# Kernel tuning notes

Hardware: AMD Instinct MI355X
Metric: run time of the kernel (lower is better)

## Reference

```python
import jax, jax.numpy as jnp
import numpy as np

B, L, D = 2, 1024, 768
NL = 8            # n_layers
DI = 2 * D        # d_inner (expand=2)
NS = 16           # d_state
DR = D // 16      # dt_rank = 48
KC = 4            # d_conv
EPS = 1e-5


def setup_inputs() -> dict:
    key = jax.random.key(0)
    ks = jax.random.split(key, 12)
    s = 0.02
    inp = {
        "x":        jax.random.normal(ks[0], (B, L, D), jnp.float32),
        "ln_w":     jnp.ones((NL, D), jnp.float32),
        "ln_b":     jnp.zeros((NL, D), jnp.float32),
        "in_proj":  jax.random.normal(ks[1], (NL, 2 * DI, D), jnp.float32) * s,
        "conv_w":   jax.random.normal(ks[2], (NL, DI, KC), jnp.float32) * 0.1,
        "conv_b":   jnp.zeros((NL, DI), jnp.float32),
        "x_proj":   jax.random.normal(ks[3], (NL, DR + 2 * NS, DI), jnp.float32) * s,
        "dt_w":     jax.random.normal(ks[4], (NL, DI, DR), jnp.float32) * s,
        "dt_b":     jax.random.normal(ks[5], (NL, DI), jnp.float32) * 0.5,
        "A_log":    jnp.broadcast_to(jnp.log(jnp.arange(1, NS + 1, dtype=jnp.float32)), (NL, DI, NS)).copy(),
        "D_skip":   jnp.ones((NL, DI), jnp.float32),
        "out_proj": jax.random.normal(ks[6], (NL, D, DI), jnp.float32) * s,
        "fn_w":     jnp.ones((D,), jnp.float32),
        "fn_b":     jnp.zeros((D,), jnp.float32),
    }
    return inp


def _layernorm(x, w, b):
    mu = x.mean(-1, keepdims=True)
    var = ((x - mu) ** 2).mean(-1, keepdims=True)
    return (x - mu) * jax.lax.rsqrt(var + EPS) * w + b


def _silu(x):
    return x * jax.nn.sigmoid(x)


def _mamba(xn, Wi, cw, cb, Wx, Wdt, bdt, A_log, Dp, Wo):
    # xn: (B, L, D)
    xz = jnp.einsum('bld,ed->ble', xn, Wi)          # (B, L, 2*DI)
    xi, z = jnp.split(xz, 2, axis=-1)               # each (B, L, DI)
    # causal depthwise conv along L
    xc = jax.lax.conv_general_dilated(
        xi.transpose(0, 2, 1), cw[:, None, :], (1,), [(KC - 1, 0)],
        feature_group_count=DI, dimension_numbers=('NCH', 'OIH', 'NCH'))
    xc = _silu(xc.transpose(0, 2, 1) + cb)          # (B, L, DI)
    dbc = jnp.einsum('ble,re->blr', xc, Wx)         # (B, L, DR+2*NS)
    dt = jax.nn.softplus(jnp.einsum('blr,dr->bld', dbc[..., :DR], Wdt) + bdt)  # (B,L,DI)
    Bm = dbc[..., DR:DR + NS]                        # (B, L, NS)
    Cm = dbc[..., DR + NS:]                          # (B, L, NS)
    A = -jnp.exp(A_log)                              # (DI, NS)

    def step(h, inp):
        dt_t, B_t, C_t, x_t = inp                    # (B,DI),(B,NS),(B,NS),(B,DI)
        dA = jnp.exp(dt_t[..., None] * A)            # (B, DI, NS)
        h = dA * h + (dt_t * x_t)[..., None] * B_t[:, None, :]
        y = jnp.einsum('bdn,bn->bd', h, C_t)
        return h, y

    xs = (dt.transpose(1, 0, 2), Bm.transpose(1, 0, 2),
          Cm.transpose(1, 0, 2), xc.transpose(1, 0, 2))
    h0 = jnp.zeros((xn.shape[0], DI, NS), xn.dtype)
    _, ys = jax.lax.scan(step, h0, xs)               # ys: (L, B, DI)
    y = ys.transpose(1, 0, 2) + xc * Dp
    y = y * _silu(z)
    return jnp.einsum('ble,de->bld', y, Wo)          # (B, L, D)


def reference(x, ln_w, ln_b, in_proj, conv_w, conv_b, x_proj, dt_w, dt_b,
              A_log, D_skip, out_proj, fn_w, fn_b):
    params = (ln_w, ln_b, in_proj, conv_w, conv_b, x_proj, dt_w, dt_b,
              A_log, D_skip, out_proj)

    def block(carry, p):
        xcur, res = carry
        lw, lb, Wi, cw, cb, Wx, Wdt, bdt, Al, Dp, Wo = p
        res = xcur + res                 # residual = x + residual
        xn = _layernorm(xcur, lw, lb)    # norm(x) -- note: norms block input, per source
        h = _mamba(xn, Wi, cw, cb, Wx, Wdt, bdt, Al, Dp, Wo)
        return (h, res), None

    res0 = jnp.zeros_like(x)             # residual=None handled as zeros
    (xf, resf), _ = jax.lax.scan(block, (x, res0), params)
    out = _layernorm(xf + resf, fn_w, fn_b)
    return out
```

## Files before the change

kernel.cpp:

```cpp
#include <hip/hip_runtime.h>
#include <math.h>

#define B_ 2
#define L_ 1024
#define D_ 768
#define NL_ 8
#define DI_ 1536
#define NS_ 16
#define DR_ 48
#define KC_ 4
#define EPS_ 1e-5f
#define M_ (B_*L_)
#define NC_ 64
#define T_ 16
#define KS_ 16
#define KCH_ (DI_/KS_)
#define KDT_ 64

typedef short bf16x8 __attribute__((ext_vector_type(8)));
typedef float f32x4  __attribute__((ext_vector_type(4)));

__device__ __forceinline__ unsigned short f2bf(float f) {
    union { float f; unsigned int u; } v; v.f = f;
    unsigned int u = v.u;
    u += 0x7fffu + ((u >> 16) & 1u);
    return (unsigned short)(u >> 16);
}

__device__ __forceinline__ unsigned int pk2(float a, float b) {
    return (unsigned int)f2bf(a) | ((unsigned int)f2bf(b) << 16);
}

__device__ __forceinline__ void gload16(const void* g, void* l) {
    __builtin_amdgcn_global_load_lds(
        (const __attribute__((address_space(1))) void*)g,
        (__attribute__((address_space(3))) void*)l, 16, 0, 0);
}

__device__ __forceinline__ void cvt16(const float* __restrict__ s,
                                      unsigned short* __restrict__ dst) {
    float4 a = *(const float4*)&s[0];
    float4 b = *(const float4*)&s[4];
    float4 c = *(const float4*)&s[8];
    float4 d = *(const float4*)&s[12];
    uint4 o0 = {pk2(a.x, a.y), pk2(a.z, a.w), pk2(b.x, b.y), pk2(b.z, b.w)};
    uint4 o1 = {pk2(c.x, c.y), pk2(c.z, c.w), pk2(d.x, d.y), pk2(d.z, d.w)};
    *(uint4*)&dst[0] = o0;
    *(uint4*)&dst[8] = o1;
}

__global__ __launch_bounds__(256) void prep_kernel(
    const float* __restrict__ wi, unsigned short* __restrict__ wi_bf,
    const float* __restrict__ wo, unsigned short* __restrict__ wo_bf,
    const float* __restrict__ wx, unsigned short* __restrict__ wx_bf,
    const float* __restrict__ wdt, unsigned short* __restrict__ wdt_bf,
    const float* __restrict__ A_log, float* __restrict__ negA,
    const float* __restrict__ x, float* __restrict__ xcur,
    float* __restrict__ res,
    unsigned short* __restrict__ dbc_bf) {
    const int E0 = NL_ * 2 * DI_ * D_;
    const int E1 = NL_ * D_ * DI_;
    const int E2 = NL_ * 80 * DI_;
    const int E3 = NL_ * DI_ * KDT_;
    const int E4 = NL_ * DI_ * NS_;
    const int E5 = M_ * D_;
    int u = (blockIdx.x * 256 + threadIdx.x) * 16;
    if (u < E0) { cvt16(&wi[u], &wi_bf[u]); return; }
    u -= E0;
    if (u < E1) { cvt16(&wo[u], &wo_bf[u]); return; }
    u -= E1;
    if (u < E2) { cvt16(&wx[u], &wx_bf[u]); return; }
    u -= E2;
    if (u < E3) {
        int col = u & (KDT_ - 1);
        if (col < DR_) {
            cvt16(&wdt[(size_t)(u >> 6) * DR_ + col], &wdt_bf[u]);
        } else {
            uint4 z = {0u, 0u, 0u, 0u};
            *(uint4*)&wdt_bf[u] = z;
            *(uint4*)&wdt_bf[u + 8] = z;
        }
        return;
    }
    u -= E3;
    if (u < E4) {
        #pragma unroll
        for (int r = 0; r < 4; r++) {
            float4 a = *(const float4*)&A_log[u + r * 4];
            float4 o = make_float4(-__expf(a.x), -__expf(a.y),
                                   -__expf(a.z), -__expf(a.w));
            *(float4*)&negA[u + r * 4] = o;
        }
        return;
    }
    u -= E4;
    if (u < E5) {
        float4 z = make_float4(0.f, 0.f, 0.f, 0.f);
        #pragma unroll
        for (int r = 0; r < 4; r++) {
            *(float4*)&xcur[u + r * 4] = *(const float4*)&x[u + r * 4];
            *(float4*)&res[u + r * 4] = z;
        }
        return;
    }
    u -= E5;
    {
        uint4 z = {0u, 0u, 0u, 0u};
        *(uint4*)&dbc_bf[u] = z;
        *(uint4*)&dbc_bf[u + 8] = z;
    }
}

__device__ __forceinline__ float block_sum256(float v) {
    __shared__ float sb[4];
    #pragma unroll
    for (int o = 32; o > 0; o >>= 1) v += __shfl_down(v, o);
    if ((threadIdx.x & 63) == 0) sb[threadIdx.x >> 6] = v;
    __syncthreads();
    float r = sb[0] + sb[1] + sb[2] + sb[3];
    __syncthreads();
    return r;
}

__global__ __launch_bounds__(256) void ln_res_kernel(
    const float* __restrict__ xcur, float* __restrict__ res,
    const float* __restrict__ w, const float* __restrict__ b,
    unsigned short* __restrict__ xn) {
    int row = blockIdx.x;
    int t = threadIdx.x;
    size_t base = (size_t)row * D_;
    float v0 = xcur[base + t];
    float v1 = xcur[base + t + 256];
    float v2 = xcur[base + t + 512];
    res[base + t]       += v0;
    res[base + t + 256] += v1;
    res[base + t + 512] += v2;
    float mu = block_sum256(v0 + v1 + v2) * (1.0f / D_);
    float d0 = v0 - mu, d1 = v1 - mu, d2 = v2 - mu;
    float var = block_sum256(d0 * d0 + d1 * d1 + d2 * d2) * (1.0f / D_);
    float rs = rsqrtf(var + EPS_);
    xn[base + t]       = f2bf(d0 * rs * w[t]       + b[t]);
    xn[base + t + 256] = f2bf(d1 * rs * w[t + 256] + b[t + 256]);
    xn[base + t + 512] = f2bf(d2 * rs * w[t + 512] + b[t + 512]);
}

__global__ __launch_bounds__(256) void final_ln_kernel(
    const float* __restrict__ xcur, const float* __restrict__ res,
    const float* __restrict__ w, const float* __restrict__ b,
    float* __restrict__ out) {
    int row = blockIdx.x;
    int t = threadIdx.x;
    size_t base = (size_t)row * D_;
    float v0 = xcur[base + t]       + res[base + t];
    float v1 = xcur[base + t + 256] + res[base + t + 256];
    float v2 = xcur[base + t + 512] + res[base + t + 512];
    float mu = block_sum256(v0 + v1 + v2) * (1.0f / D_);
    float d0 = v0 - mu, d1 = v1 - mu, d2 = v2 - mu;
    float var = block_sum256(d0 * d0 + d1 * d1 + d2 * d2) * (1.0f / D_);
    float rs = rsqrtf(var + EPS_);
    out[base + t]       = d0 * rs * w[t]       + b[t];
    out[base + t + 256] = d1 * rs * w[t + 256] + b[t + 256];
    out[base + t + 512] = d2 * rs * w[t + 512] + b[t + 512];
}

template <int BM, int BN>
__global__ __launch_bounds__(256) void gemm_bf16_t(
    const unsigned short* __restrict__ A,
    const unsigned short* __restrict__ W,
    float* __restrict__ C, int M, int N, int K) {
    constexpr int FM = BM / 32;
    constexpr int FN = BN / 32;
    constexpr int NLD = (BM + BN) / 64;
    __shared__ unsigned short sA[BM * 32];
    __shared__ unsigned short sW[BN * 32];
    int bm = blockIdx.y * BM, bn = blockIdx.x * BN;
    int tid = threadIdx.x;
    int wave = tid >> 6, lane = tid & 63;
    int wrow = (wave & 1) * (BM / 2), wcol = (wave >> 1) * (BN / 2);
    int quad = lane >> 4, r16 = lane & 15;
    f32x4 acc[FM][FN];
    #pragma unroll
    for (int i = 0; i < FM; i++)
        #pragma unroll
        for (int j = 0; j < FN; j++)
            acc[i][j] = (f32x4){0.f, 0.f, 0.f, 0.f};

    for (int k0 = 0; k0 < K; k0 += 32) {
        #pragma unroll
        for (int r = 0; r < NLD; r++) {
            if (r < BM / 64) {
                int j = r * 256 + tid;
                gload16(&A[(size_t)(bm + (j >> 2)) * K + k0 + (j & 3) * 8],
                        &sA[(r * 256 + wave * 64) * 8]);
            } else {
                int j = (r - BM / 64) * 256 + tid;
                gload16(&W[(size_t)(bn + (j >> 2)) * K + k0 + (j & 3) * 8],
                        &sW[((r - BM / 64) * 256 + wave * 64) * 8]);
            }
        }
        __syncthreads();
        bf16x8 af[FM], wf[FN];
        #pragma unroll
        for (int i = 0; i < FM; i++)
            af[i] = *(const bf16x8*)&sA[(wrow + i * 16 + r16) * 32 + quad * 8];
        #pragma unroll
        for (int j = 0; j < FN; j++)
            wf[j] = *(const bf16x8*)&sW[(wcol + j * 16 + r16) * 32 + quad * 8];
        #pragma unroll
        for (int i = 0; i < FM; i++)
            #pragma unroll
            for (int j = 0; j < FN; j++)
                acc[i][j] = __builtin_amdgcn_mfma_f32_16x16x32_bf16(
                    af[i], wf[j], acc[i][j], 0, 0, 0);
        __syncthreads();
    }
    #pragma unroll
    for (int i = 0; i < FM; i++) {
        #pragma unroll
        for (int j = 0; j < FN; j++) {
            int col = bn + wcol + j * 16 + r16;
            #pragma unroll
            for (int reg = 0; reg < 4; reg++) {
                int row = bm + wrow + i * 16 + quad * 4 + reg;
                C[(size_t)row * N + col] = acc[i][j][reg];
            }
        }
    }
}

__global__ __launch_bounds__(256) void dt_gemm_bf16(
    const unsigned short* __restrict__ A,
    const unsigned short* __restrict__ W,
    const float* __restrict__ bias,
    float* __restrict__ dtb) {
    __shared__ unsigned short sA[128 * 32];
    __shared__ unsigned short sW[128 * 32];
    int bm = blockIdx.y * 128, bn = blockIdx.x * 128;
    int tid = threadIdx.x;
    int wave = tid >> 6, lane = tid & 63;
    int wrow = (wave & 1) * 64, wcol = (wave >> 1) * 64;
    int quad = lane >> 4, r16 = lane & 15;
    f32x4 acc[4][4];
    #pragma unroll
    for (int i = 0; i < 4; i++)
        #pragma unroll
        for (int j = 0; j < 4; j++)
            acc[i][j] = (f32x4){0.f, 0.f, 0.f, 0.f};

    #pragma unroll
    for (int k0 = 0; k0 < KDT_; k0 += 32) {
        #pragma unroll
        for (int r = 0; r < 4; r++) {
            if (r < 2) {
                int j = r * 256 + tid;
                gload16(&A[(size_t)(bm + (j >> 2)) * KDT_ + k0 + (j & 3) * 8],
                        &sA[(r * 256 + wave * 64) * 8]);
            } else {
                int j = (r - 2) * 256 + tid;
                gload16(&W[(size_t)(bn + (j >> 2)) * KDT_ + k0 + (j & 3) * 8],
                        &sW[((r - 2) * 256 + wave * 64) * 8]);
            }
        }
        __syncthreads();
        bf16x8 af[4], wf[4];
        #pragma unroll
        for (int i = 0; i < 4; i++)
            af[i] = *(const bf16x8*)&sA[(wrow + i * 16 + r16) * 32 + quad * 8];
        #pragma unroll
        for (int j = 0; j < 4; j++)
            wf[j] = *(const bf16x8*)&sW[(wcol + j * 16 + r16) * 32 + quad * 8];
        #pragma unroll
        for (int i = 0; i < 4; i++)
            #pragma unroll
            for (int j = 0; j < 4; j++)
                acc[i][j] = __builtin_amdgcn_mfma_f32_16x16x32_bf16(
                    af[i], wf[j], acc[i][j], 0, 0, 0);
        __syncthreads();
    }
    #pragma unroll
    for (int i = 0; i < 4; i++) {
        #pragma unroll
        for (int j = 0; j < 4; j++) {
            int col = bn + wcol + j * 16 + r16;
            float bv = bias[col];
            #pragma unroll
            for (int reg = 0; reg < 4; reg++) {
                int row = bm + wrow + i * 16 + quad * 4 + reg;
                float v = acc[i][j][reg] + bv;
                v = (v > 20.f) ? v : log1pf(__expf(v));
                dtb[(size_t)row * DI_ + col] = v;
            }
        }
    }
}

__global__ __launch_bounds__(256) void xproj_gemm_kernel(
    const unsigned short* __restrict__ A,
    const unsigned short* __restrict__ W,
    float* __restrict__ Pb) {
    __shared__ unsigned short sA[64 * 32];
    __shared__ unsigned short sW[80 * 32];
    int ks = blockIdx.x;
    int bm = blockIdx.y * 64;
    int tid = threadIdx.x;
    int wave = tid >> 6, lane = tid & 63;
    int quad = lane >> 4, r16 = lane & 15;
    f32x4 acc[5];
    #pragma unroll
    for (int j = 0; j < 5; j++) acc[j] = (f32x4){0.f, 0.f, 0.f, 0.f};
    int k0base = ks * KCH_;
    for (int kc = 0; kc < KCH_; kc += 32) {
        int k0 = k0base + kc;
        gload16(&A[(size_t)(bm + (tid >> 2)) * DI_ + k0 + (tid & 3) * 8],
                &sA[wave * 512]);
        gload16(&W[(size_t)(tid >> 2) * DI_ + k0 + (tid & 3) * 8],
                &sW[wave * 512]);
        if (tid < 64) {
            int c = 256 + tid;
            gload16(&W[(size_t)(c >> 2) * DI_ + k0 + (c & 3) * 8],
                    &sW[2048]);
        }
        __syncthreads();
        bf16x8 af = *(const bf16x8*)&sA[(wave * 16 + r16) * 32 + quad * 8];
        #pragma unroll
        for (int j = 0; j < 5; j++) {
            bf16x8 wf = *(const bf16x8*)&sW[(j * 16 + r16) * 32 + quad * 8];
            acc[j] = __builtin_amdgcn_mfma_f32_16x16x32_bf16(af, wf, acc[j], 0, 0, 0);
        }
        __syncthreads();
    }
    #pragma unroll
    for (int j = 0; j < 5; j++) {
        int col = j * 16 + r16;
        #pragma unroll
        for (int reg = 0; reg < 4; reg++) {
            int row = bm + wave * 16 + quad * 4 + reg;
            Pb[((size_t)ks * M_ + row) * 80 + col] = acc[j][reg];
        }
    }
}

__global__ void xproj_reduce_kernel(const float* __restrict__ Pb,
                                    unsigned short* __restrict__ dbc_bf,
                                    float* __restrict__ bcp) {
    int i = blockIdx.x * 256 + threadIdx.x;
    float s = 0.f;
    #pragma unroll
    for (int ks = 0; ks < KS_; ks++) s += Pb[(size_t)ks * (M_ * 80) + i];
    int m = i / 80, col = i % 80;
    if (col < DR_) {
        dbc_bf[m * KDT_ + col] = f2bf(s);
    } else if (col < DR_ + NS_) {
        bcp[m * 32 + 2 * (col - DR_)] = s;
    } else {
        bcp[m * 32 + 2 * (col - DR_ - NS_) + 1] = s;
    }
}

__global__ __launch_bounds__(256) void conv_silu_kernel(
    const float* __restrict__ xz,
    const float* __restrict__ cw,
    const float* __restrict__ cb,
    float* __restrict__ xcf,
    unsigned short* __restrict__ xcb) {
    int idx = blockIdx.x * 256 + threadIdx.x;
    int d = idx % DI_;
    int t4 = (idx / DI_) % (L_ / 4);
    int b = idx / (DI_ * (L_ / 4));
    int t0 = t4 * 4;
    float4 wv = *(const float4*)&cw[d * KC_];
    float bias = cb[d];
    float xs[7];
    #pragma unroll
    for (int k = 0; k < 7; k++) {
        int tt = t0 - 3 + k;
        xs[k] = (tt >= 0) ? xz[((size_t)(b * L_ + tt)) * (2 * DI_) + d] : 0.f;
    }
    #pragma unroll
    for (int r = 0; r < 4; r++) {
        float acc = bias + xs[r] * wv.x + xs[r + 1] * wv.y
                         + xs[r + 2] * wv.z + xs[r + 3] * wv.w;
        float v = acc / (1.0f + __expf(-acc));
        size_t row = (size_t)(b * L_ + t0 + r);
        xcf[row * DI_ + d] = v;
        xcb[row * DI_ + d] = f2bf(v);
    }
}

__global__ __launch_bounds__(256) void scan_ps_kernel(
    const float* __restrict__ dtb,
    const float* __restrict__ xcf,
    const float4* __restrict__ bcp4,
    const float* __restrict__ negA,
    float2* __restrict__ PS) {
    const int NDB = DI_ / 256;
    int bx = blockIdx.x;
    int dblk = bx % NDB;
    int c = (bx / NDB) % NC_;
    int b = bx / (NDB * NC_);
    int d = dblk * 256 + threadIdx.x;

    float A[NS_];
    #pragma unroll
    for (int n = 0; n < NS_; n++) A[n] = negA[(size_t)d * NS_ + n];
    float h[NS_];
    #pragma unroll
    for (int n = 0; n < NS_; n++) h[n] = 0.f;
    float sd = 0.f;

    size_t btbase = (size_t)(b * L_ + c * T_);
    const float* pdt = dtb + btbase * DI_ + d;
    const float* pxc = xcf + btbase * DI_ + d;
    const float4* pbc = bcp4 + btbase * 8;

    #pragma unroll
    for (int t = 0; t < T_; t++) {
        float dt = pdt[(size_t)t * DI_];
        float u  = dt * pxc[(size_t)t * DI_];
        sd += dt;
        #pragma unroll
        for (int q = 0; q < 8; q++) {
            float4 v = pbc[t * 8 + q];
            float e0 = __expf(dt * A[2 * q]);
            h[2 * q] = fmaf(e0, h[2 * q], u * v.x);
            float e1 = __expf(dt * A[2 * q + 1]);
            h[2 * q + 1] = fmaf(e1, h[2 * q + 1], u * v.z);
        }
    }

    size_t o = (((size_t)b * NC_ + c) * DI_ + d) * NS_;
    #pragma unroll
    for (int n = 0; n < NS_; n++)
        PS[o + n] = make_float2(__expf(A[n] * sd), h[n]);
}

__global__ __launch_bounds__(256) void scan_combine_kernel(
    const float2* __restrict__ PS, float* __restrict__ hin) {
    int i = blockIdx.x * 256 + threadIdx.x;
    int b = i / (DI_ * NS_);
    int rem = i % (DI_ * NS_);
    const size_t str = (size_t)DI_ * NS_;
    size_t o = (size_t)b * NC_ * str + rem;
    float h = 0.f;
    float2 ps = PS[o];
    #pragma unroll 4
    for (int c = 0; c < NC_ - 1; c++) {
        float2 psn = PS[o + str];
        hin[o] = h;
        h = fmaf(ps.x, h, ps.y);
        ps = psn;
        o += str;
    }
    hin[o] = h;
}

__global__ __launch_bounds__(256) void scan_out_kernel(
    const float* __restrict__ dtb, const float* __restrict__ xcf,
    const float4* __restrict__ bcp4, const float* __restrict__ negA,
    const float* __restrict__ hin, const float* __restrict__ xz,
    const float* __restrict__ Dp, unsigned short* __restrict__ yg) {
    const int NDB = DI_ / 256;
    int bx = blockIdx.x;
    int dblk = bx % NDB;
    int c = (bx / NDB) % NC_;
    int b = bx / (NDB * NC_);
    int d = dblk * 256 + threadIdx.x;

    float A[NS_];
    #pragma unroll
    for (int n = 0; n < NS_; n++) A[n] = negA[(size_t)d * NS_ + n];
    size_t o = (((size_t)b * NC_ + c) * DI_ + d) * NS_;
    float h[NS_];
    #pragma unroll
    for (int n = 0; n < NS_; n++) h[n] = hin[o + n];
    float dpv = Dp[d];

    size_t btbase = (size_t)(b * L_ + c * T_);
    const float* pdt = dtb + btbase * DI_ + d;
    const float* pxc = xcf + btbase * DI_ + d;
    const float4* pbc = bcp4 + btbase * 8;

    #pragma unroll
    for (int t = 0; t < T_; t++) {
        float dt = pdt[(size_t)t * DI_];
        float xc = pxc[(size_t)t * DI_];
        float u = dt * xc;
        float y = 0.f;
        #pragma unroll
        for (int q = 0; q < 8; q++) {
            float4 v = pbc[t * 8 + q];
            float e0 = __expf(dt * A[2 * q]);
            h[2 * q] = fmaf(e0, h[2 * q], u * v.x);
            y = fmaf(v.y, h[2 * q], y);
            float e1 = __expf(dt * A[2 * q + 1]);
            h[2 * q + 1] = fmaf(e1, h[2 * q + 1], u * v.z);
            y = fmaf(v.w, h[2 * q + 1], y);
        }
        size_t row = btbase + t;
        float zv = xz[row * (2 * DI_) + DI_ + d];
        float yy = y + xc * dpv;
        yy *= zv / (1.0f + __expf(-zv));
        yg[row * DI_ + d] = f2bf(yy);
    }
}

extern "C" void kernel_launch(void* const* d_in, const int* in_sizes, int n_in,
                              void* d_out, int out_size, void* d_ws, size_t ws_size,
                              hipStream_t stream) {
    const float* x        = (const float*)d_in[0];
    const float* ln_w     = (const float*)d_in[1];
    const float* ln_b     = (const float*)d_in[2];
    const float* in_proj  = (const float*)d_in[3];
    const float* conv_w   = (const float*)d_in[4];
    const float* conv_b   = (const float*)d_in[5];
    const float* x_proj   = (const float*)d_in[6];
    const float* dt_w     = (const float*)d_in[7];
    const float* dt_b     = (const float*)d_in[8];
    const float* A_log    = (const float*)d_in[9];
    const float* D_skip   = (const float*)d_in[10];
    const float* out_proj = (const float*)d_in[11];
    const float* fn_w     = (const float*)d_in[12];
    const float* fn_b     = (const float*)d_in[13];
    float* out = (float*)d_out;

    char* p = (char*)d_ws;
    auto alloc = [&](size_t bytes) {
        char* r = p;
        p += (bytes + 255) & ~(size_t)255;
        return (void*)r;
    };
    float* xcur = (float*)alloc((size_t)M_ * D_ * 4);
    float* res  = (float*)alloc((size_t)M_ * D_ * 4);
    unsigned short* xn = (unsigned short*)alloc((size_t)M_ * D_ * 2);
    float* xz   = (float*)alloc((size_t)M_ * 2 * DI_ * 4);
    unsigned short* xcb = (unsigned short*)alloc((size_t)M_ * DI_ * 2);
    float* dtb  = (float*)alloc((size_t)M_ * DI_ * 4);
    float* xcf  = (float*)alloc((size_t)M_ * DI_ * 4);
    unsigned short* dbc_bf = (unsigned short*)alloc((size_t)M_ * KDT_ * 2);
    float* bcp  = (float*)alloc((size_t)M_ * 32 * 4);
    unsigned short* yg = (unsigned short*)alloc((size_t)M_ * DI_ * 2);
    float2* PS  = (float2*)alloc((size_t)B_ * NC_ * DI_ * NS_ * 8);
    float* hin  = (float*)alloc((size_t)B_ * NC_ * DI_ * NS_ * 4);
    float* Pb   = (float*)alloc((size_t)KS_ * M_ * 80 * 4);
    float* negA = (float*)alloc((size_t)NL_ * DI_ * NS_ * 4);
    const size_t n_wi = (size_t)NL_ * 2 * DI_ * D_;
    const size_t n_wo = (size_t)NL_ * D_ * DI_;
    const size_t n_wx = (size_t)NL_ * 80 * DI_;
    const size_t n_wdt = (size_t)NL_ * DI_ * KDT_;
    unsigned short* wi_bf = (unsigned short*)alloc(n_wi * 2);
    unsigned short* wo_bf = (unsigned short*)alloc(n_wo * 2);
    unsigned short* wx_bf = (unsigned short*)alloc(n_wx * 2);
    unsigned short* wdt_bf = (unsigned short*)alloc(n_wdt * 2);

    prep_kernel<<<7808, 256, 0, stream>>>(
        in_proj, wi_bf, out_proj, wo_bf, x_proj, wx_bf,
        dt_w, wdt_bf, A_log, negA, x, xcur, res, dbc_bf);

    for (int l = 0; l < NL_; l++) {
        const float* negA_l = negA + (size_t)l * DI_ * NS_;

        ln_res_kernel<<<M_, 256, 0, stream>>>(
            xcur, res, ln_w + l * D_, ln_b + l * D_, xn);

        gemm_bf16_t<128, 128><<<dim3((2 * DI_) / 128, M_ / 128), 256, 0, stream>>>(
            xn, wi_bf + (size_t)l * 2 * DI_ * D_, xz, M_, 2 * DI_, D_);

        conv_silu_kernel<<<(B_ * (L_ / 4) * DI_) / 256, 256, 0, stream>>>(
            xz, conv_w + l * DI_ * KC_, conv_b + l * DI_, xcf, xcb);

        xproj_gemm_kernel<<<dim3(KS_, M_ / 64), 256, 0, stream>>>(
            xcb, wx_bf + (size_t)l * 80 * DI_, Pb);
        xproj_reduce_kernel<<<(M_ * 80) / 256, 256, 0, stream>>>(Pb, dbc_bf, bcp);

        dt_gemm_bf16<<<dim3(DI_ / 128, M_ / 128), 256, 0, stream>>>(
            dbc_bf, wdt_bf + (size_t)l * DI_ * KDT_, dt_b + l * DI_, dtb);

        scan_ps_kernel<<<B_ * NC_ * (DI_ / 256), 256, 0, stream>>>(
            dtb, xcf, (const float4*)bcp, negA_l, PS);
        scan_combine_kernel<<<(B_ * DI_ * NS_) / 256, 256, 0, stream>>>(PS, hin);
        scan_out_kernel<<<B_ * NC_ * (DI_ / 256), 256, 0, stream>>>(
            dtb, xcf, (const float4*)bcp, negA_l, hin, xz,
            D_skip + (size_t)l * DI_, yg);

        gemm_bf16_t<128, 64><<<dim3(D_ / 64, M_ / 128), 256, 0, stream>>>(
            yg, wo_bf + (size_t)l * D_ * DI_, xcur, M_, D_, DI_);
    }

    final_ln_kernel<<<M_, 256, 0, stream>>>(xcur, res, fn_w, fn_b, out);
}
```

Baseline: 1.441 ms.

## Fuse conv+SiLU into x_proj GEMM and shrink scan chunk-state traffic

Folds the causal depthwise conv and SiLU into the split-K x_proj GEMM kernel. Each block builds its bf16 activation tile in shared memory, so the bf16 xc buffer is no longer written and read back. The scan prefix pass now stores only the chunk state h and the summed dt per channel, and the combine kernel recomputes the decay exp(A*sum_dt), which shrinks the chunk-state traffic. Weight prep is also restructured for coalesced per-block conversion. The trade-offs are extra shared memory per block (less occupancy) and redundant exp work in the combine kernel.

```diff
diff --git a/kernel.cpp b/kernel.cpp
--- a/kernel.cpp
+++ b/kernel.cpp
@@ -28,7 +28,11 @@
 }
 
 __device__ __forceinline__ unsigned int pk2(float a, float b) {
-    return (unsigned int)f2bf(a) | ((unsigned int)f2bf(b) << 16);
+    union { float f; unsigned int u; } va, vb;
+    va.f = a; vb.f = b;
+    unsigned int ua = va.u + (0x7fffu + ((va.u >> 16) & 1u));
+    unsigned int ub = vb.u + (0x7fffu + ((vb.u >> 16) & 1u));
+    return (ua >> 16) | (ub & 0xffff0000u);
 }
 
 __device__ __forceinline__ void gload16(const void* g, void* l) {
@@ -37,16 +41,15 @@
         (__attribute__((address_space(3))) void*)l, 16, 0, 0);
 }
 
-__device__ __forceinline__ void cvt16(const float* __restrict__ s,
-                                      unsigned short* __restrict__ dst) {
-    float4 a = *(const float4*)&s[0];
-    float4 b = *(const float4*)&s[4];
-    float4 c = *(const float4*)&s[8];
-    float4 d = *(const float4*)&s[12];
-    uint4 o0 = {pk2(a.x, a.y), pk2(a.z, a.w), pk2(b.x, b.y), pk2(b.z, b.w)};
-    uint4 o1 = {pk2(c.x, c.y), pk2(c.z, c.w), pk2(d.x, d.y), pk2(d.z, d.w)};
-    *(uint4*)&dst[0] = o0;
-    *(uint4*)&dst[8] = o1;
+__device__ __forceinline__ void cvt_blk(const float* __restrict__ s,
+                                        unsigned short* __restrict__ d, int tid) {
+    #pragma unroll
+    for (int r = 0; r < 4; r++) {
+        int off = tid * 4 + r * 1024;
+        float4 a = *(const float4*)&s[off];
+        uint2 o = {pk2(a.x, a.y), pk2(a.z, a.w)};
+        *(uint2*)&d[off] = o;
+    }
 }
 
 __global__ __launch_bounds__(256) void prep_kernel(
@@ -64,50 +67,58 @@
     const int E3 = NL_ * DI_ * KDT_;
     const int E4 = NL_ * DI_ * NS_;
     const int E5 = M_ * D_;
-    int u = (blockIdx.x * 256 + threadIdx.x) * 16;
-    if (u < E0) { cvt16(&wi[u], &wi_bf[u]); return; }
-    u -= E0;
-    if (u < E1) { cvt16(&wo[u], &wo_bf[u]); return; }
-    u -= E1;
-    if (u < E2) { cvt16(&wx[u], &wx_bf[u]); return; }
-    u -= E2;
-    if (u < E3) {
-        int col = u & (KDT_ - 1);
-        if (col < DR_) {
-            cvt16(&wdt[(size_t)(u >> 6) * DR_ + col], &wdt_bf[u]);
-        } else {
-            uint4 z = {0u, 0u, 0u, 0u};
-            *(uint4*)&wdt_bf[u] = z;
-            *(uint4*)&wdt_bf[u + 8] = z;
+    int tid = threadIdx.x;
+    int base = blockIdx.x * 4096;
+    if (base < E0) { cvt_blk(wi + base, wi_bf + base, tid); return; }
+    base -= E0;
+    if (base < E1) { cvt_blk(wo + base, wo_bf + base, tid); return; }
+    base -= E1;
+    if (base < E2) { cvt_blk(wx + base, wx_bf + base, tid); return; }
+    base -= E2;
+    if (base < E3) {
+        #pragma unroll
+        for (int r = 0; r < 4; r++) {
+            int off = base + tid * 4 + r * 1024;
+            int col = off & (KDT_ - 1);
+            uint2 o = {0u, 0u};
+            if (col < DR_) {
+                float4 a = *(const float4*)&wdt[(size_t)(off >> 6) * DR_ + col];
+                o = (uint2){pk2(a.x, a.y), pk2(a.z, a.w)};
+            }
+            *(uint2*)&wdt_bf[off] = o;
         }
         return;
     }
-    u -= E3;
-    if (u < E4) {
+    base -= E3;
+    if (base < E4) {
         #pragma unroll
         for (int r = 0; r < 4; r++) {
-            float4 a = *(const float4*)&A_log[u + r * 4];
+            int off = base + tid * 4 + r * 1024;
+            float4 a = *(const float4*)&A_log[off];
             float4 o = make_float4(-__expf(a.x), -__expf(a.y),
                                    -__expf(a.z), -__expf(a.w));
-            *(float4*)&negA[u + r * 4] = o;
+            *(float4*)&negA[off] = o;
         }
         return;
     }
-    u -= E4;
-    if (u < E5) {
+    base -= E4;
+    if (base < E5) {
         float4 z = make_float4(0.f, 0.f, 0.f, 0.f);
         #pragma unroll
         for (int r = 0; r < 4; r++) {
-            *(float4*)&xcur[u + r * 4] = *(const float4*)&x[u + r * 4];
-            *(float4*)&res[u + r * 4] = z;
+            int off = base + tid * 4 + r * 1024;
+            *(float4*)&xcur[off] = *(const float4*)&x[off];
+            *(float4*)&res[off] = z;
         }
         return;
     }
-    u -= E5;
+    base -= E5;
     {
-        uint4 z = {0u, 0u, 0u, 0u};
-        *(uint4*)&dbc_bf[u] = z;
-        *(uint4*)&dbc_bf[u + 8] = z;
+        #pragma unroll
+        for (int r = 0; r < 4; r++) {
+            int off = base + tid * 4 + r * 1024;
+            *(uint2*)&dbc_bf[off] = (uint2){0u, 0u};
+        }
     }
 }
 
@@ -294,40 +305,69 @@
     }
 }
 
-__global__ __launch_bounds__(256) void xproj_gemm_kernel(
-    const unsigned short* __restrict__ A,
+__global__ __launch_bounds__(256) void conv_xproj_kernel(
+    const float* __restrict__ xz,
+    const float* __restrict__ cw,
+    const float* __restrict__ cb,
     const unsigned short* __restrict__ W,
+    float* __restrict__ xcf,
     float* __restrict__ Pb) {
-    __shared__ unsigned short sA[64 * 32];
-    __shared__ unsigned short sW[80 * 32];
+    __shared__ float sxz[67 * 96];
+    __shared__ unsigned short sxcb[64 * 104];
+    __shared__ float scw[96 * 4];
+    __shared__ float scb[96];
+    unsigned short* sW = (unsigned short*)sxz;
+
     int ks = blockIdx.x;
     int bm = blockIdx.y * 64;
     int tid = threadIdx.x;
+    int b = bm >> 10, t0 = bm & (L_ - 1);
+    int dbase = ks * KCH_;
+
+    if (tid < 96) {
+        int d = dbase + tid;
+        *(float4*)&scw[tid * 4] = *(const float4*)&cw[d * 4];
+        scb[tid] = cb[d];
+    }
+    for (int j = tid; j < 67 * 24; j += 256) {
+        int r = j / 24, c4 = (j % 24) * 4;
+        int tt = t0 + r - 3;
+        float4 v = make_float4(0.f, 0.f, 0.f, 0.f);
+        if (tt >= 0)
+            v = *(const float4*)&xz[((size_t)(b * L_ + tt)) * (2 * DI_) + dbase + c4];
+        *(float4*)&sxz[r * 96 + c4] = v;
+    }
+    __syncthreads();
+    for (int j = tid; j < 64 * 96; j += 256) {
+        int r = j / 96, c = j % 96;
+        float acc = scb[c];
+        #pragma unroll
+        for (int k = 0; k < KC_; k++)
+            acc = fmaf(scw[c * 4 + k], sxz[(r + k) * 96 + c], acc);
+        float v = acc / (1.0f + __expf(-acc));
+        xcf[(size_t)(bm + r) * DI_ + dbase + c] = v;
+        sxcb[r * 104 + c] = f2bf(v);
+    }
+    __syncthreads();
+    for (int j = tid; j < 80 * 12; j += 256) {
+        int row = j / 12, c16 = (j % 12) * 8;
+        *(uint4*)&sW[row * 104 + c16] =
+            *(const uint4*)&W[(size_t)row * DI_ + dbase + c16];
+    }
+    __syncthreads();
     int wave = tid >> 6, lane = tid & 63;
     int quad = lane >> 4, r16 = lane & 15;
     f32x4 acc[5];
     #pragma unroll
     for (int j = 0; j < 5; j++) acc[j] = (f32x4){0.f, 0.f, 0.f, 0.f};
-    int k0base = ks * KCH_;
-    for (int kc = 0; kc < KCH_; kc += 32) {
-        int k0 = k0base + kc;
-        gload16(&A[(size_t)(bm + (tid >> 2)) * DI_ + k0 + (tid & 3) * 8],
-                &sA[wave * 512]);
-        gload16(&W[(size_t)(tid >> 2) * DI_ + k0 + (tid & 3) * 8],
-                &sW[wave * 512]);
-        if (tid < 64) {
-            int c = 256 + tid;
-            gload16(&W[(size_t)(c >> 2) * DI_ + k0 + (c & 3) * 8],
-                    &sW[2048]);
-        }
-        __syncthreads();
-        bf16x8 af = *(const bf16x8*)&sA[(wave * 16 + r16) * 32 + quad * 8];
+    #pragma unroll
+    for (int kk = 0; kk < 3; kk++) {
+        bf16x8 af = *(const bf16x8*)&sxcb[(wave * 16 + r16) * 104 + kk * 32 + quad * 8];
         #pragma unroll
         for (int j = 0; j < 5; j++) {
-            bf16x8 wf = *(const bf16x8*)&sW[(j * 16 + r16) * 32 + quad * 8];
+            bf16x8 wf = *(const bf16x8*)&sW[(j * 16 + r16) * 104 + kk * 32 + quad * 8];
             acc[j] = __builtin_amdgcn_mfma_f32_16x16x32_bf16(af, wf, acc[j], 0, 0, 0);
         }
-        __syncthreads();
     }
     #pragma unroll
     for (int j = 0; j < 5; j++) {
@@ -357,42 +397,13 @@
     }
 }
 
-__global__ __launch_bounds__(256) void conv_silu_kernel(
-    const float* __restrict__ xz,
-    const float* __restrict__ cw,
-    const float* __restrict__ cb,
-    float* __restrict__ xcf,
-    unsigned short* __restrict__ xcb) {
-    int idx = blockIdx.x * 256 + threadIdx.x;
-    int d = idx % DI_;
-    int t4 = (idx / DI_) % (L_ / 4);
-    int b = idx / (DI_ * (L_ / 4));
-    int t0 = t4 * 4;
-    float4 wv = *(const float4*)&cw[d * KC_];
-    float bias = cb[d];
-    float xs[7];
-    #pragma unroll
-    for (int k = 0; k < 7; k++) {
-        int tt = t0 - 3 + k;
-        xs[k] = (tt >= 0) ? xz[((size_t)(b * L_ + tt)) * (2 * DI_) + d] : 0.f;
-    }
-    #pragma unroll
-    for (int r = 0; r < 4; r++) {
-        float acc = bias + xs[r] * wv.x + xs[r + 1] * wv.y
-                         + xs[r + 2] * wv.z + xs[r + 3] * wv.w;
-        float v = acc / (1.0f + __expf(-acc));
-        size_t row = (size_t)(b * L_ + t0 + r);
-        xcf[row * DI_ + d] = v;
-        xcb[row * DI_ + d] = f2bf(v);
-    }
-}
-
 __global__ __launch_bounds__(256) void scan_ps_kernel(
     const float* __restrict__ dtb,
     const float* __restrict__ xcf,
     const float4* __restrict__ bcp4,
     const float* __restrict__ negA,
-    float2* __restrict__ PS) {
+    float* __restrict__ Sb,
+    float* __restrict__ sdb) {
     const int NDB = DI_ / 256;
     int bx = blockIdx.x;
     int dblk = bx % NDB;
@@ -430,26 +441,31 @@
 
     size_t o = (((size_t)b * NC_ + c) * DI_ + d) * NS_;
     #pragma unroll
-    for (int n = 0; n < NS_; n++)
-        PS[o + n] = make_float2(__expf(A[n] * sd), h[n]);
+    for (int n = 0; n < NS_; n++) Sb[o + n] = h[n];
+    sdb[((size_t)b * NC_ + c) * DI_ + d] = sd;
 }
 
 __global__ __launch_bounds__(256) void scan_combine_kernel(
-    const float2* __restrict__ PS, float* __restrict__ hin) {
+    const float* __restrict__ Sb, const float* __restrict__ sdb,
+    const float* __restrict__ negA, float* __restrict__ hin) {
     int i = blockIdx.x * 256 + threadIdx.x;
     int b = i / (DI_ * NS_);
     int rem = i % (DI_ * NS_);
+    int d = rem >> 4;
+    float Aa = negA[rem];
     const size_t str = (size_t)DI_ * NS_;
     size_t o = (size_t)b * NC_ * str + rem;
+    size_t osd = (size_t)b * NC_ * DI_ + d;
     float h = 0.f;
-    float2 ps = PS[o];
+    float s = Sb[o], sd = sdb[osd];
     #pragma unroll 4
     for (int c = 0; c < NC_ - 1; c++) {
-        float2 psn = PS[o + str];
+        float sn = Sb[o + str];
+        float sdn = sdb[osd + DI_];
         hin[o] = h;
-        h = fmaf(ps.x, h, ps.y);
-        ps = psn;
-        o += str;
+        h = fmaf(__expf(Aa * sd), h, s);
+        s = sn; sd = sdn;
+        o += str; osd += DI_;
     }
     hin[o] = h;
 }
@@ -533,13 +549,13 @@
     float* res  = (float*)alloc((size_t)M_ * D_ * 4);
     unsigned short* xn = (unsigned short*)alloc((size_t)M_ * D_ * 2);
     float* xz   = (float*)alloc((size_t)M_ * 2 * DI_ * 4);
-    unsigned short* xcb = (unsigned short*)alloc((size_t)M_ * DI_ * 2);
     float* dtb  = (float*)alloc((size_t)M_ * DI_ * 4);
     float* xcf  = (float*)alloc((size_t)M_ * DI_ * 4);
     unsigned short* dbc_bf = (unsigned short*)alloc((size_t)M_ * KDT_ * 2);
     float* bcp  = (float*)alloc((size_t)M_ * 32 * 4);
     unsigned short* yg = (unsigned short*)alloc((size_t)M_ * DI_ * 2);
-    float2* PS  = (float2*)alloc((size_t)B_ * NC_ * DI_ * NS_ * 8);
+    float* Sb   = (float*)alloc((size_t)B_ * NC_ * DI_ * NS_ * 4);
+    float* sdb  = (float*)alloc((size_t)B_ * NC_ * DI_ * 4);
     float* hin  = (float*)alloc((size_t)B_ * NC_ * DI_ * NS_ * 4);
     float* Pb   = (float*)alloc((size_t)KS_ * M_ * 80 * 4);
     float* negA = (float*)alloc((size_t)NL_ * DI_ * NS_ * 4);
@@ -565,19 +581,18 @@
         gemm_bf16_t<128, 128><<<dim3((2 * DI_) / 128, M_ / 128), 256, 0, stream>>>(
             xn, wi_bf + (size_t)l * 2 * DI_ * D_, xz, M_, 2 * DI_, D_);
 
-        conv_silu_kernel<<<(B_ * (L_ / 4) * DI_) / 256, 256, 0, stream>>>(
-            xz, conv_w + l * DI_ * KC_, conv_b + l * DI_, xcf, xcb);
-
-        xproj_gemm_kernel<<<dim3(KS_, M_ / 64), 256, 0, stream>>>(
-            xcb, wx_bf + (size_t)l * 80 * DI_, Pb);
+        conv_xproj_kernel<<<dim3(KS_, M_ / 64), 256, 0, stream>>>(
+            xz, conv_w + l * DI_ * KC_, conv_b + l * DI_,
+            wx_bf + (size_t)l * 80 * DI_, xcf, Pb);
         xproj_reduce_kernel<<<(M_ * 80) / 256, 256, 0, stream>>>(Pb, dbc_bf, bcp);
 
         dt_gemm_bf16<<<dim3(DI_ / 128, M_ / 128), 256, 0, stream>>>(
             dbc_bf, wdt_bf + (size_t)l * DI_ * KDT_, dt_b + l * DI_, dtb);
 
         scan_ps_kernel<<<B_ * NC_ * (DI_ / 256), 256, 0, stream>>>(
-            dtb, xcf, (const float4*)bcp, negA_l, PS);
-        scan_combine_kernel<<<(B_ * DI_ * NS_) / 256, 256, 0, stream>>>(PS, hin);
+            dtb, xcf, (const float4*)bcp, negA_l, Sb, sdb);
+        scan_combine_kernel<<<(B_ * DI_ * NS_) / 256, 256, 0, stream>>>(
+            Sb, sdb, negA_l, hin);
         scan_out_kernel<<<B_ * NC_ * (DI_ / 256), 256, 0, stream>>>(
             dtb, xcf, (const float4*)bcp, negA_l, hin, xz,
             D_skip + (size_t)l * DI_, yg);
```

After: 1.408 ms. 2.4% less time.
